# Optimization experiments

Hardware: AMD Instinct MI355X
Metric: run time of the kernel (lower is better)

Reference implementation:

```python
import jax, jax.numpy as jnp
import numpy as np

N_NODES = 50000
N_EDGES = 800000
IN_FEATS = 128
OUT_FEATS = 128
HEADS = 2
EW_DIMS = 2
NEG_SLOPE = 0.2


def setup_inputs() -> dict:
    key = jax.random.key(0)
    ks = jax.random.split(key, 8)
    feat = jax.random.normal(ks[0], (N_NODES, IN_FEATS), dtype=jnp.float32)
    e_w = jax.random.uniform(ks[1], (N_EDGES, EW_DIMS), dtype=jnp.float32)
    src = jax.random.randint(ks[2], (N_EDGES,), 0, N_NODES)
    dst = jax.random.randint(ks[3], (N_EDGES,), 0, N_NODES)
    # Learned params: per-head fc weight, attn vectors (xavier-ish scale)
    s = 1.0 / np.sqrt(IN_FEATS)
    W = jax.random.normal(ks[4], (HEADS, OUT_FEATS, IN_FEATS), dtype=jnp.float32) * s
    attn_l = jax.random.normal(ks[5], (HEADS, OUT_FEATS), dtype=jnp.float32) * s
    attn_r = jax.random.normal(ks[6], (HEADS, OUT_FEATS), dtype=jnp.float32) * s
    attn_ew = jax.random.normal(ks[7], (HEADS, EW_DIMS), dtype=jnp.float32)
    return {"feat": feat, "e_w": e_w, "src": src, "dst": dst,
            "W": W, "attn_l": attn_l, "attn_r": attn_r, "attn_ew": attn_ew}


def reference(feat, e_w, src, dst, W, attn_l, attn_r, attn_ew):
    N = feat.shape[0]
    # per-head projection: [N, H, O]
    ft = jnp.einsum('nf,hof->nho', feat, W)
    el = jnp.einsum('nho,ho->nh', ft, attn_l)           # [N, H]
    er = jnp.einsum('nho,ho->nh', ft, attn_r)           # [N, H]
    ew = jnp.einsum('ed,hd->eh', e_w, attn_ew)          # [E, H]
    # u_add_v + edge-weight attention + leaky_relu
    e = jax.nn.leaky_relu(el[src] + er[dst] + ew, NEG_SLOPE)  # [E, H]
    # edge_softmax grouped by destination node (numerically stable)
    emax = jax.ops.segment_max(e, dst, num_segments=N)
    emax = jnp.where(jnp.isfinite(emax), emax, 0.0)
    ee = jnp.exp(e - emax[dst])
    denom = jax.ops.segment_sum(ee, dst, num_segments=N)
    a = ee / jnp.where(denom[dst] > 0, denom[dst], 1.0)       # [E, H]
    # u_mul_e / sum aggregation: [N, H, O]
    m = ft[src] * a[:, :, None]
    rst = jax.ops.segment_sum(m, dst, num_segments=N)
    # residual (Identity since in_feats == out_feats) + elu, then cat heads
    rst = jax.nn.elu(rst + feat[:, None, :])
    return rst.reshape(N, -1)
```

## Files before the change

### kernel.cpp

```cpp
#include <hip/hip_runtime.h>
#include <hip/hip_bf16.h>
#include <math.h>

#define NNODES 50000
#define NEDGES 800000
#define INF 128
#define OUTF 128
#define HEADS 2
#define NEG_SLOPE 0.2f

#define CAP 32
#define OVFCAP 32768

__device__ __forceinline__ unsigned short f2bf(float f) {
    unsigned u = __float_as_uint(f);
    unsigned r = (u + 0x7FFFu + ((u >> 16) & 1u)) >> 16;
    return (unsigned short)r;
}
__device__ __forceinline__ float bf2f(unsigned short b) {
    return __uint_as_float((unsigned)b << 16);
}

typedef __attribute__((ext_vector_type(8))) short frag_ab;
typedef __attribute__((ext_vector_type(4))) float frag_cd;

#define APITCH 136

__global__ void init_kernel(int* cursor, int* ovfcnt, int N) {
    int i = blockIdx.x * 256 + threadIdx.x;
    if (i < N) cursor[i] = 0;
    if (i == 0) *ovfcnt = 0;
}

__global__ __launch_bounds__(256) void gemm_mfma(const float* __restrict__ feat,
                                                 const float* __restrict__ W,
                                                 const float* __restrict__ attn_l,
                                                 const float* __restrict__ attn_r,
                                                 unsigned short* __restrict__ ftb,
                                                 float* __restrict__ elp,
                                                 float* __restrict__ erp,
                                                 int N) {
    __shared__ unsigned short Asl[64 * APITCH];
    __shared__ unsigned short Bsl[64 * APITCH];
    const int t = threadIdx.x;
    const int n0 = blockIdx.x * 64;
    const int w = t >> 6, lane = t & 63;
    const int m16 = lane & 15, quad = lane >> 4;

#pragma unroll
    for (int i = 0; i < 8; ++i) {
        int q = t + i * 256;
        int r = q >> 5;
        int c4 = q & 31;
        int gn = n0 + r;
        float4 g = (gn < N) ? *(const float4*)(feat + (size_t)gn * INF + c4 * 4)
                            : make_float4(0.f, 0.f, 0.f, 0.f);
        ushort4 v; v.x = f2bf(g.x); v.y = f2bf(g.y); v.z = f2bf(g.z); v.w = f2bf(g.w);
        *(ushort4*)(&Asl[r * APITCH + c4 * 4]) = v;
    }

    const int arow = w * 16 + m16;

    for (int jt = 0; jt < 4; ++jt) {
        __syncthreads();
#pragma unroll
        for (int i = 0; i < 8; ++i) {
            int q = t + i * 256;
            int r = q >> 5;
            int c4 = q & 31;
            float4 g = *(const float4*)(W + (size_t)(jt * 64 + r) * INF + c4 * 4);
            ushort4 v; v.x = f2bf(g.x); v.y = f2bf(g.y); v.z = f2bf(g.z); v.w = f2bf(g.w);
            *(ushort4*)(&Bsl[r * APITCH + c4 * 4]) = v;
        }
        __syncthreads();

        frag_cd acc[4];
#pragma unroll
        for (int nt = 0; nt < 4; ++nt) acc[nt] = frag_cd{0.f, 0.f, 0.f, 0.f};

#pragma unroll
        for (int kc = 0; kc < 4; ++kc) {
            frag_ab af = *(frag_ab*)(&Asl[arow * APITCH + kc * 32 + quad * 8]);
#pragma unroll
            for (int nt = 0; nt < 4; ++nt) {
                frag_ab bf = *(frag_ab*)(&Bsl[(nt * 16 + m16) * APITCH + kc * 32 + quad * 8]);
                acc[nt] = __builtin_amdgcn_mfma_f32_16x16x32_bf16(af, bf, acc[nt], 0, 0, 0);
            }
        }

        float pl[4] = {0.f, 0.f, 0.f, 0.f};
        float pr[4] = {0.f, 0.f, 0.f, 0.f};
#pragma unroll
        for (int nt = 0; nt < 4; ++nt) {
            int gj = jt * 64 + nt * 16 + m16;
            float a_l = attn_l[gj];
            float a_r = attn_r[gj];
#pragma unroll
            for (int reg = 0; reg < 4; ++reg) {
                float val = acc[nt][reg];
                pl[reg] += val * a_l;
                pr[reg] += val * a_r;
                int gm = n0 + w * 16 + quad * 4 + reg;
                if (gm < N)
                    ftb[(size_t)gm * 256 + gj] = f2bf(val);
            }
        }
#pragma unroll
        for (int m = 1; m < 16; m <<= 1) {
#pragma unroll
            for (int reg = 0; reg < 4; ++reg) {
                pl[reg] += __shfl_xor(pl[reg], m, 64);
                pr[reg] += __shfl_xor(pr[reg], m, 64);
            }
        }
        if (m16 == 0) {
#pragma unroll
            for (int reg = 0; reg < 4; ++reg) {
                int gm = n0 + w * 16 + quad * 4 + reg;
                if (gm < N) {
                    elp[(size_t)gm * 4 + jt] = pl[reg];
                    erp[(size_t)gm * 4 + jt] = pr[reg];
                }
            }
        }
    }
}

__global__ void edge_fused(const float* __restrict__ elp, const float* __restrict__ erp,
                           const float* __restrict__ e_w, const int* __restrict__ src,
                           const int* __restrict__ dst, const float* __restrict__ attn_ew,
                           int* __restrict__ cursor, int* __restrict__ ovfcnt,
                           uint2* __restrict__ edata, float4* __restrict__ ovf,
                           int E) {
    int e = blockIdx.x * 256 + threadIdx.x;
    if (e >= E) return;
    int s = src[e], d = dst[e];
    float2 ew2 = *(const float2*)(e_w + (size_t)e * 2);
    float4 elv = *(const float4*)(elp + (size_t)s * 4);
    float4 erv = *(const float4*)(erp + (size_t)d * 4);
    float v0 = (elv.x + elv.y) + (erv.x + erv.y) + ew2.x * attn_ew[0] + ew2.y * attn_ew[1];
    float v1 = (elv.z + elv.w) + (erv.z + erv.w) + ew2.x * attn_ew[2] + ew2.y * attn_ew[3];
    v0 = v0 >= 0.f ? v0 : NEG_SLOPE * v0;
    v1 = v1 >= 0.f ? v1 : NEG_SLOPE * v1;
    float ee0 = __expf(v0);
    float ee1 = __expf(v1);
    int pos = atomicAdd(cursor + d, 1);
    if (pos < CAP) {
        unsigned pk = ((unsigned)f2bf(ee1) << 16) | (unsigned)f2bf(ee0);
        edata[(size_t)d * CAP + pos] = make_uint2((unsigned)s, pk);
    } else {
        int o = atomicAdd(ovfcnt, 1);
        if (o < OVFCAP)
            ovf[o] = make_float4(__int_as_float(d), __int_as_float(s), ee0, ee1);
    }
}

__global__ __launch_bounds__(256) void aggregate(const unsigned short* __restrict__ ftb,
                                                 const float* __restrict__ feat,
                                                 const uint2* __restrict__ edata,
                                                 const int* __restrict__ cursor,
                                                 const int* __restrict__ ovfcnt,
                                                 const float4* __restrict__ ovf,
                                                 float* __restrict__ out, int N) {
    const int t = threadIdx.x;
    const int w = t >> 6, l = t & 63;
    const int n = blockIdx.x * 4 + w;
    if (n >= N) return;
    const int c0 = 4 * l;
    const int h = l >> 5;
    const int cnt = cursor[n];
    const int cmain = cnt < CAP ? cnt : CAP;
    const uint2* eb = edata + (size_t)n * CAP;

    float4 acc = make_float4(0.f, 0.f, 0.f, 0.f);
    float dn = 0.f;
#pragma unroll 4
    for (int i = 0; i < cmain; ++i) {
        uint2 rec = eb[i];
        int s = (int)rec.x;
        float a = bf2f((unsigned short)(h ? (rec.y >> 16) : (rec.y & 0xFFFFu)));
        dn += a;
        ushort4 v = *(const ushort4*)(ftb + (size_t)s * 256 + c0);
        acc.x += a * bf2f(v.x);
        acc.y += a * bf2f(v.y);
        acc.z += a * bf2f(v.z);
        acc.w += a * bf2f(v.w);
    }
    if (cnt > CAP) {
        int no = *ovfcnt; if (no > OVFCAP) no = OVFCAP;
        for (int i = 0; i < no; ++i) {
            float4 ov = ovf[i];
            if (__float_as_int(ov.x) == n) {
                int s = __float_as_int(ov.y);
                float a = h ? ov.w : ov.z;
                dn += a;
                ushort4 v = *(const ushort4*)(ftb + (size_t)s * 256 + c0);
                acc.x += a * bf2f(v.x);
                acc.y += a * bf2f(v.y);
                acc.z += a * bf2f(v.z);
                acc.w += a * bf2f(v.w);
            }
        }
    }
    float inv = dn > 0.f ? 1.0f / dn : 0.f;
    float4 f4 = *(const float4*)(feat + (size_t)n * INF + (c0 & 127));
    float4 r;
    r.x = acc.x * inv + f4.x;
    r.y = acc.y * inv + f4.y;
    r.z = acc.z * inv + f4.z;
    r.w = acc.w * inv + f4.w;
    r.x = r.x > 0.f ? r.x : expm1f(r.x);
    r.y = r.y > 0.f ? r.y : expm1f(r.y);
    r.z = r.z > 0.f ? r.z : expm1f(r.z);
    r.w = r.w > 0.f ? r.w : expm1f(r.w);
    *(float4*)(out + (size_t)n * 256 + c0) = r;
}

extern "C" void kernel_launch(void* const* d_in, const int* in_sizes, int n_in,
                              void* d_out, int out_size, void* d_ws, size_t ws_size,
                              hipStream_t stream) {
    const float* feat    = (const float*)d_in[0];
    const float* e_w     = (const float*)d_in[1];
    const int*   src     = (const int*)d_in[2];
    const int*   dst     = (const int*)d_in[3];
    const float* W       = (const float*)d_in[4];
    const float* attn_l  = (const float*)d_in[5];
    const float* attn_r  = (const float*)d_in[6];
    const float* attn_ew = (const float*)d_in[7];
    float* out = (float*)d_out;

    const int N = in_sizes[0] / INF;
    const int E = in_sizes[2];

    unsigned short* ftb = (unsigned short*)d_ws;
    uint2*  edata  = (uint2*)(ftb + (size_t)N * 256);
    float*  elp    = (float*)(edata + (size_t)N * CAP);
    float*  erp    = elp + (size_t)N * 4;
    float4* ovf    = (float4*)(erp + (size_t)N * 4);
    int*    cursor = (int*)(ovf + OVFCAP);
    int*    ovfcnt = cursor + N;

    init_kernel<<<(N + 255) / 256, 256, 0, stream>>>(cursor, ovfcnt, N);

    gemm_mfma<<<(N + 63) / 64, 256, 0, stream>>>(feat, W, attn_l, attn_r, ftb, elp, erp, N);

    edge_fused<<<(E + 255) / 256, 256, 0, stream>>>(elp, erp, e_w, src, dst, attn_ew,
                                                    cursor, ovfcnt, edata, ovf, E);

    aggregate<<<(N + 3) / 4, 256, 0, stream>>>(ftb, feat, edata, cursor, ovfcnt, ovf, out, N);
}
```

Before: 220.3 us.

## Fold attention vectors into W, pre-convert W to bf16, broadcast edge records via readlane

Precomputes W^T·attn_l/attn_r and a bf16 copy of W in the init kernel, so the GEMM computes el/er as direct dot products with feat and reads B fragments straight from global memory without LDS staging or barriers. The aggregate kernel loads each node's edge records once into lanes and broadcasts them with readlane, removing a dependent load per edge, and switches to fmaf. This trades shared-memory reuse of W for L2 reads and slightly changes the numerics of el/er (computed in fp32 on feat rather than on bf16-rounded ft).

Measured after the change: 251.3 us. 14.1% more time.

```diff
diff --git a/kernel.cpp b/kernel.cpp
--- a/kernel.cpp
+++ b/kernel.cpp
@@ -1,5 +1,4 @@
 #include <hip/hip_runtime.h>
-#include <hip/hip_bf16.h>
 #include <math.h>
 
 #define NNODES 50000
@@ -24,109 +23,115 @@
 typedef __attribute__((ext_vector_type(8))) short frag_ab;
 typedef __attribute__((ext_vector_type(4))) float frag_cd;
 
-#define APITCH 136
-
-__global__ void init_kernel(int* cursor, int* ovfcnt, int N) {
-    int i = blockIdx.x * 256 + threadIdx.x;
-    if (i < N) cursor[i] = 0;
-    if (i == 0) *ovfcnt = 0;
+__global__ void init_kernel(int* cursor, int* ovfcnt,
+                            const float* __restrict__ W,
+                            const float* __restrict__ attn_l,
+                            const float* __restrict__ attn_r,
+                            unsigned short* __restrict__ Wb,
+                            float* __restrict__ wfold, int N) {
+    const int b = blockIdx.x, t = threadIdx.x;
+    const int cblk = (N + 255) >> 8;
+    if (b < cblk) {
+        int i = b * 256 + t;
+        if (i < N) cursor[i] = 0;
+        if (i == 0) *ovfcnt = 0;
+        return;
+    }
+    if (b == cblk) {
+        int h = t >> 7, f = t & 127;
+        float sl = 0.f, sr = 0.f;
+        for (int o = 0; o < 128; ++o) {
+            float wv = W[(size_t)(h * 128 + o) * 128 + f];
+            sl = fmaf(attn_l[h * 128 + o], wv, sl);
+            sr = fmaf(attn_r[h * 128 + o], wv, sr);
+        }
+        wfold[h * 128 + f] = sl;
+        wfold[(2 + h) * 128 + f] = sr;
+        return;
+    }
+    int base = (b - cblk - 1) * 4096 + t * 16;
+#pragma unroll
+    for (int q = 0; q < 4; ++q) {
+        float4 g = *(const float4*)(W + base + q * 4);
+        ushort4 v; v.x = f2bf(g.x); v.y = f2bf(g.y); v.z = f2bf(g.z); v.w = f2bf(g.w);
+        *(ushort4*)(Wb + base + q * 4) = v;
+    }
 }
 
 __global__ __launch_bounds__(256) void gemm_mfma(const float* __restrict__ feat,
-                                                 const float* __restrict__ W,
-                                                 const float* __restrict__ attn_l,
-                                                 const float* __restrict__ attn_r,
+                                                 const unsigned short* __restrict__ Wb,
+                                                 const float* __restrict__ wfold,
                                                  unsigned short* __restrict__ ftb,
-                                                 float* __restrict__ elp,
-                                                 float* __restrict__ erp,
+                                                 float* __restrict__ el,
+                                                 float* __restrict__ er,
                                                  int N) {
-    __shared__ unsigned short Asl[64 * APITCH];
-    __shared__ unsigned short Bsl[64 * APITCH];
     const int t = threadIdx.x;
-    const int n0 = blockIdx.x * 64;
     const int w = t >> 6, lane = t & 63;
     const int m16 = lane & 15, quad = lane >> 4;
-
-#pragma unroll
-    for (int i = 0; i < 8; ++i) {
-        int q = t + i * 256;
-        int r = q >> 5;
-        int c4 = q & 31;
-        int gn = n0 + r;
-        float4 g = (gn < N) ? *(const float4*)(feat + (size_t)gn * INF + c4 * 4)
-                            : make_float4(0.f, 0.f, 0.f, 0.f);
-        ushort4 v; v.x = f2bf(g.x); v.y = f2bf(g.y); v.z = f2bf(g.z); v.w = f2bf(g.w);
-        *(ushort4*)(&Asl[r * APITCH + c4 * 4]) = v;
-    }
-
-    const int arow = w * 16 + m16;
-
+    const int n0 = blockIdx.x * 64;
+    const int r = n0 + w * 16 + m16;
+    const bool valid = r < N;
+
+    frag_ab af[4];
+    float pd[4] = {0.f, 0.f, 0.f, 0.f};
+#pragma unroll
+    for (int kc = 0; kc < 4; ++kc) {
+        const int cc = kc * 32 + quad * 8;
+        float4 g0 = make_float4(0.f, 0.f, 0.f, 0.f), g1 = g0;
+        if (valid) {
+            g0 = *(const float4*)(feat + (size_t)r * INF + cc);
+            g1 = *(const float4*)(feat + (size_t)r * INF + cc + 4);
+        }
+        frag_ab a;
+        a[0] = (short)f2bf(g0.x); a[1] = (short)f2bf(g0.y);
+        a[2] = (short)f2bf(g0.z); a[3] = (short)f2bf(g0.w);
+        a[4] = (short)f2bf(g1.x); a[5] = (short)f2bf(g1.y);
+        a[6] = (short)f2bf(g1.z); a[7] = (short)f2bf(g1.w);
+        af[kc] = a;
+#pragma unroll
+        for (int vq = 0; vq < 4; ++vq) {
+            float4 w0 = *(const float4*)(wfold + vq * 128 + cc);
+            float4 w1 = *(const float4*)(wfold + vq * 128 + cc + 4);
+            pd[vq] += g0.x * w0.x + g0.y * w0.y + g0.z * w0.z + g0.w * w0.w
+                    + g1.x * w1.x + g1.y * w1.y + g1.z * w1.z + g1.w * w1.w;
+        }
+    }
+#pragma unroll
+    for (int m = 16; m < 64; m <<= 1)
+#pragma unroll
+        for (int vq = 0; vq < 4; ++vq) pd[vq] += __shfl_xor(pd[vq], m, 64);
+    if (valid && quad == 0) {
+        *(float2*)(el + (size_t)r * 2) = make_float2(pd[0], pd[1]);
+        *(float2*)(er + (size_t)r * 2) = make_float2(pd[2], pd[3]);
+    }
+
+#pragma unroll
     for (int jt = 0; jt < 4; ++jt) {
-        __syncthreads();
-#pragma unroll
-        for (int i = 0; i < 8; ++i) {
-            int q = t + i * 256;
-            int r = q >> 5;
-            int c4 = q & 31;
-            float4 g = *(const float4*)(W + (size_t)(jt * 64 + r) * INF + c4 * 4);
-            ushort4 v; v.x = f2bf(g.x); v.y = f2bf(g.y); v.z = f2bf(g.z); v.w = f2bf(g.w);
-            *(ushort4*)(&Bsl[r * APITCH + c4 * 4]) = v;
-        }
-        __syncthreads();
-
         frag_cd acc[4];
 #pragma unroll
         for (int nt = 0; nt < 4; ++nt) acc[nt] = frag_cd{0.f, 0.f, 0.f, 0.f};
-
 #pragma unroll
         for (int kc = 0; kc < 4; ++kc) {
-            frag_ab af = *(frag_ab*)(&Asl[arow * APITCH + kc * 32 + quad * 8]);
 #pragma unroll
             for (int nt = 0; nt < 4; ++nt) {
-                frag_ab bf = *(frag_ab*)(&Bsl[(nt * 16 + m16) * APITCH + kc * 32 + quad * 8]);
-                acc[nt] = __builtin_amdgcn_mfma_f32_16x16x32_bf16(af, bf, acc[nt], 0, 0, 0);
+                frag_ab bf = *(const frag_ab*)(Wb + (size_t)(jt * 64 + nt * 16 + m16) * INF
+                                               + kc * 32 + quad * 8);
+                acc[nt] = __builtin_amdgcn_mfma_f32_16x16x32_bf16(af[kc], bf, acc[nt], 0, 0, 0);
             }
         }
-
-        float pl[4] = {0.f, 0.f, 0.f, 0.f};
-        float pr[4] = {0.f, 0.f, 0.f, 0.f};
 #pragma unroll
         for (int nt = 0; nt < 4; ++nt) {
-            int gj = jt * 64 + nt * 16 + m16;
-            float a_l = attn_l[gj];
-            float a_r = attn_r[gj];
-#pragma unroll
-            for (int reg = 0; reg < 4; ++reg) {
-                float val = acc[nt][reg];
-                pl[reg] += val * a_l;
-                pr[reg] += val * a_r;
-                int gm = n0 + w * 16 + quad * 4 + reg;
-                if (gm < N)
-                    ftb[(size_t)gm * 256 + gj] = f2bf(val);
-            }
-        }
-#pragma unroll
-        for (int m = 1; m < 16; m <<= 1) {
-#pragma unroll
-            for (int reg = 0; reg < 4; ++reg) {
-                pl[reg] += __shfl_xor(pl[reg], m, 64);
-                pr[reg] += __shfl_xor(pr[reg], m, 64);
-            }
-        }
-        if (m16 == 0) {
+            const int gj = jt * 64 + nt * 16 + m16;
 #pragma unroll
             for (int reg = 0; reg < 4; ++reg) {
                 int gm = n0 + w * 16 + quad * 4 + reg;
-                if (gm < N) {
-                    elp[(size_t)gm * 4 + jt] = pl[reg];
-                    erp[(size_t)gm * 4 + jt] = pr[reg];
-                }
+                if (gm < N) ftb[(size_t)gm * 256 + gj] = f2bf(acc[nt][reg]);
             }
         }
     }
 }
 
-__global__ void edge_fused(const float* __restrict__ elp, const float* __restrict__ erp,
+__global__ void edge_fused(const float* __restrict__ el, const float* __restrict__ er,
                            const float* __restrict__ e_w, const int* __restrict__ src,
                            const int* __restrict__ dst, const float* __restrict__ attn_ew,
                            int* __restrict__ cursor, int* __restrict__ ovfcnt,
@@ -136,10 +141,10 @@
     if (e >= E) return;
     int s = src[e], d = dst[e];
     float2 ew2 = *(const float2*)(e_w + (size_t)e * 2);
-    float4 elv = *(const float4*)(elp + (size_t)s * 4);
-    float4 erv = *(const float4*)(erp + (size_t)d * 4);
-    float v0 = (elv.x + elv.y) + (erv.x + erv.y) + ew2.x * attn_ew[0] + ew2.y * attn_ew[1];
-    float v1 = (elv.z + elv.w) + (erv.z + erv.w) + ew2.x * attn_ew[2] + ew2.y * attn_ew[3];
+    float2 elv = *(const float2*)(el + (size_t)s * 2);
+    float2 erv = *(const float2*)(er + (size_t)d * 2);
+    float v0 = elv.x + erv.x + ew2.x * attn_ew[0] + ew2.y * attn_ew[1];
+    float v1 = elv.y + erv.y + ew2.x * attn_ew[2] + ew2.y * attn_ew[3];
     v0 = v0 >= 0.f ? v0 : NEG_SLOPE * v0;
     v1 = v1 >= 0.f ? v1 : NEG_SLOPE * v1;
     float ee0 = __expf(v0);
@@ -171,20 +176,21 @@
     const int cnt = cursor[n];
     const int cmain = cnt < CAP ? cnt : CAP;
     const uint2* eb = edata + (size_t)n * CAP;
+    const uint2 myrec = eb[l & 31];
 
     float4 acc = make_float4(0.f, 0.f, 0.f, 0.f);
     float dn = 0.f;
 #pragma unroll 4
     for (int i = 0; i < cmain; ++i) {
-        uint2 rec = eb[i];
-        int s = (int)rec.x;
-        float a = bf2f((unsigned short)(h ? (rec.y >> 16) : (rec.y & 0xFFFFu)));
+        unsigned sx = (unsigned)__builtin_amdgcn_readlane((int)myrec.x, i);
+        unsigned pk = (unsigned)__builtin_amdgcn_readlane((int)myrec.y, i);
+        float a = bf2f((unsigned short)(h ? (pk >> 16) : (pk & 0xFFFFu)));
+        const ushort4 v = *(const ushort4*)(ftb + (size_t)sx * 256 + c0);
         dn += a;
-        ushort4 v = *(const ushort4*)(ftb + (size_t)s * 256 + c0);
-        acc.x += a * bf2f(v.x);
-        acc.y += a * bf2f(v.y);
-        acc.z += a * bf2f(v.z);
-        acc.w += a * bf2f(v.w);
+        acc.x = fmaf(a, bf2f(v.x), acc.x);
+        acc.y = fmaf(a, bf2f(v.y), acc.y);
+        acc.z = fmaf(a, bf2f(v.z), acc.z);
+        acc.w = fmaf(a, bf2f(v.w), acc.w);
     }
     if (cnt > CAP) {
         int no = *ovfcnt; if (no > OVFCAP) no = OVFCAP;
@@ -194,11 +200,11 @@
                 int s = __float_as_int(ov.y);
                 float a = h ? ov.w : ov.z;
                 dn += a;
-                ushort4 v = *(const ushort4*)(ftb + (size_t)s * 256 + c0);
-                acc.x += a * bf2f(v.x);
-                acc.y += a * bf2f(v.y);
-                acc.z += a * bf2f(v.z);
-                acc.w += a * bf2f(v.w);
+                const ushort4 v = *(const ushort4*)(ftb + (size_t)s * 256 + c0);
+                acc.x = fmaf(a, bf2f(v.x), acc.x);
+                acc.y = fmaf(a, bf2f(v.y), acc.y);
+                acc.z = fmaf(a, bf2f(v.z), acc.z);
+                acc.w = fmaf(a, bf2f(v.w), acc.w);
             }
         }
     }
@@ -234,17 +240,20 @@
 
     unsigned short* ftb = (unsigned short*)d_ws;
     uint2*  edata  = (uint2*)(ftb + (size_t)N * 256);
-    float*  elp    = (float*)(edata + (size_t)N * CAP);
-    float*  erp    = elp + (size_t)N * 4;
-    float4* ovf    = (float4*)(erp + (size_t)N * 4);
+    float*  el     = (float*)(edata + (size_t)N * CAP);
+    float*  er     = el + (size_t)N * 2;
+    float*  wfold  = er + (size_t)N * 2;
+    unsigned short* Wb = (unsigned short*)(wfold + 512);
+    float4* ovf    = (float4*)(Wb + 32768);
     int*    cursor = (int*)(ovf + OVFCAP);
     int*    ovfcnt = cursor + N;
 
-    init_kernel<<<(N + 255) / 256, 256, 0, stream>>>(cursor, ovfcnt, N);
-
-    gemm_mfma<<<(N + 63) / 64, 256, 0, stream>>>(feat, W, attn_l, attn_r, ftb, elp, erp, N);
-
-    edge_fused<<<(E + 255) / 256, 256, 0, stream>>>(elp, erp, e_w, src, dst, attn_ew,
+    const int cblk = (N + 255) / 256;
+    init_kernel<<<cblk + 9, 256, 0, stream>>>(cursor, ovfcnt, W, attn_l, attn_r, Wb, wfold, N);
+
+    gemm_mfma<<<(N + 63) / 64, 256, 0, stream>>>(feat, Wb, wfold, ftb, el, er, N);
+
+    edge_fused<<<(E + 255) / 256, 256, 0, stream>>>(el, er, e_w, src, dst, attn_ew,
                                                     cursor, ovfcnt, edata, ovf, E);
 
     aggregate<<<(N + 3) / 4, 256, 0, stream>>>(ftb, feat, edata, cursor, ovfcnt, ovf, out, N);
```
